# Kernel tuning notes

Hardware: AMD Instinct MI355X
Metric: run time of the kernel (lower is better)

## Reference

```python
import jax, jax.numpy as jnp
import numpy as np

NEG_SLOPE = 0.2  # negative_slope of LeakyReLU

def _leaky_relu(x):
    return jnp.where(x >= 0, x, NEG_SLOPE * x)

def setup_inputs() -> dict:
    key = jax.random.key(0)
    ks = jax.random.split(key, 8)
    n_s, n_t, n_edges = 100000, 25000, 1600000
    d_s_in = d_t_in = 256
    d_s_out = d_t_out = 256
    x_source = jax.random.normal(ks[0], (n_s, d_s_in), jnp.float32)
    x_target = jax.random.normal(ks[1], (n_t, d_t_in), jnp.float32)
    # sparse neighborhood N: [n_target, n_source], COO (row=target i, col=source j)
    edge_row = jax.random.randint(ks[2], (n_edges,), 0, n_t)
    edge_col = jax.random.randint(ks[3], (n_edges,), 0, n_s)
    n_vals = jax.random.uniform(ks[4], (n_edges,), jnp.float32)
    # learnable parameters (xavier-uniform-ish scale)
    w_s = jax.random.normal(ks[5], (d_s_in, d_t_out), jnp.float32) * 0.074  # [source_in, target_out]
    w_t = jax.random.normal(ks[6], (d_t_in, d_s_out), jnp.float32) * 0.074  # [target_in, source_out]
    att_weight = jax.random.normal(ks[7], (d_t_out + d_s_out,), jnp.float32) * 0.074
    return {"x_source": x_source, "x_target": x_target, "n_vals": n_vals,
            "w_s": w_s, "w_t": w_t, "att_weight": att_weight,
            "edge_row": edge_row, "edge_col": edge_col}

def reference(x_source, x_target, n_vals, w_s, w_t, att_weight, edge_row, edge_col):
    n_s = x_source.shape[0]
    n_t = x_target.shape[0]
    d_t_out = w_s.shape[1]  # target_out_channels (split point of att_weight)
    s_msg = x_source @ w_s  # [n_s, target_out]
    t_msg = x_target @ w_t  # [n_t, source_out]
    # e_ij = LeakyReLU([s_msg_j || t_msg_i] @ a); factor the linear part per node
    a1 = att_weight[:d_t_out]   # acts on s_msg part
    a2 = att_weight[d_t_out:]   # acts on t_msg part
    p_s = s_msg @ a1            # [n_s]
    p_t = t_msg @ a2            # [n_t]
    # f on the transposed edge (i'=source=col, j'=target=row) with permuted weight
    # [a2 || a1] gives p_t[row] + p_s[col]: identical per-edge scores as e.
    ev = _leaky_relu(p_s[edge_col] + p_t[edge_row])  # [E]
    # sparse_row_norm (softmax=False): divide by row sums
    rowsum_t = jax.ops.segment_sum(ev, edge_row, num_segments=n_t)  # rows of N
    rowsum_s = jax.ops.segment_sum(ev, edge_col, num_segments=n_s)  # rows of N^T
    att_s = ev / rowsum_t[edge_row]  # A_s, aligned with N
    att_t = ev / rowsum_s[edge_col]  # A_t, aligned with N^T
    # Hadamard with N values, then sparse-dense matmul (scatter-add)
    w_e = n_vals * att_s
    w_f = n_vals * att_t
    message_on_target = jax.ops.segment_sum(w_e[:, None] * s_msg[edge_col], edge_row, num_segments=n_t)  # Y_t
    message_on_source = jax.ops.segment_sum(w_f[:, None] * t_msg[edge_row], edge_col, num_segments=n_s)  # Y_s
    # update_func=None -> identity
    return message_on_source, message_on_target
```

## Files before the change

### kernel.cpp

```cpp
#include <hip/hip_runtime.h>

#define D 256

typedef float f32x4 __attribute__((ext_vector_type(4)));
typedef unsigned int u32x2 __attribute__((ext_vector_type(2)));
typedef short bf16x8 __attribute__((ext_vector_type(8)));
typedef float floatx4 __attribute__((ext_vector_type(4)));

__device__ __forceinline__ unsigned int rne_bf16(float f) {
    unsigned int u = __float_as_uint(f);
    return (u + 0x7FFFu + ((u >> 16) & 1u)) >> 16;
}

#define PROWS 32
#define PSTRIDE (D + 4)

__global__ __launch_bounds__(256) void fused_p_all(
        const float* __restrict__ xs, const float* __restrict__ ws,
        float* __restrict__ ps, unsigned short* __restrict__ xbs, int n_s, int nblk_s,
        const float* __restrict__ xt, const float* __restrict__ wt,
        float* __restrict__ pt, unsigned short* __restrict__ xbt, int n_t,
        const float* __restrict__ att) {
    __shared__ float sbuf[PROWS][PSTRIDE];
    const float* X; const float* W; float* p; unsigned short* xb;
    int M, att_off, row0;
    if (blockIdx.x < (unsigned)nblk_s) {
        X = xs; W = ws; p = ps; xb = xbs; M = n_s; att_off = 0;
        row0 = blockIdx.x * PROWS;
    } else {
        X = xt; W = wt; p = pt; xb = xbt; M = n_t; att_off = D;
        row0 = (blockIdx.x - nblk_s) * PROWS;
    }
    const int tid = threadIdx.x;
    for (int idx = tid; idx < PROWS * (D / 4); idx += 256) {
        int r = idx >> 6;
        int c4 = (idx & 63) * 4;
        int grow = row0 + r;
        int srcrow = grow < M ? grow : M - 1;
        *reinterpret_cast<float4*>(&sbuf[r][c4]) =
            *reinterpret_cast<const float4*>(X + (size_t)srcrow * D + c4);
    }
    __syncthreads();

    if (xb) {
        const int half = tid >> 7;
        const int c2 = (tid & 127) * 2;
        for (int r = half; r < PROWS; r += 2) {
            int row = row0 + r;
            if (row < M) {
                unsigned int u0 = rne_bf16(sbuf[r][c2]);
                unsigned int u1 = rne_bf16(sbuf[r][c2 + 1]);
                *reinterpret_cast<unsigned int*>(xb + (size_t)row * D + c2) =
                    (u1 << 16) | u0;
            }
        }
    }

    const int g = tid >> 6;
    const int l = tid & 63;
    const int r0 = g * 8;
    float acc[8][4];
    #pragma unroll
    for (int r = 0; r < 8; ++r)
        #pragma unroll
        for (int q = 0; q < 4; ++q) acc[r][q] = 0.f;

    const float* wbase = W + 4 * l;
    for (int k8 = 0; k8 < D; k8 += 8) {
        float4 wv[8];
        #pragma unroll
        for (int kk = 0; kk < 8; ++kk)
            wv[kk] = *reinterpret_cast<const float4*>(wbase + (size_t)(k8 + kk) * D);
        #pragma unroll
        for (int h = 0; h < 2; ++h) {
            float4 xv[8];
            #pragma unroll
            for (int r = 0; r < 8; ++r)
                xv[r] = *reinterpret_cast<const float4*>(&sbuf[r0 + r][k8 + 4 * h]);
            #pragma unroll
            for (int kk = 0; kk < 4; ++kk) {
                float4 w4 = wv[4 * h + kk];
                #pragma unroll
                for (int r = 0; r < 8; ++r) {
                    float xsc = (kk == 0) ? xv[r].x : (kk == 1) ? xv[r].y
                              : (kk == 2) ? xv[r].z : xv[r].w;
                    acc[r][0] = __fmaf_rn(xsc, w4.x, acc[r][0]);
                    acc[r][1] = __fmaf_rn(xsc, w4.y, acc[r][1]);
                    acc[r][2] = __fmaf_rn(xsc, w4.z, acc[r][2]);
                    acc[r][3] = __fmaf_rn(xsc, w4.w, acc[r][3]);
                }
            }
        }
    }
    __syncthreads();
    #pragma unroll
    for (int r = 0; r < 8; ++r)
        *reinterpret_cast<float4*>(&sbuf[r0 + r][4 * l]) =
            make_float4(acc[r][0], acc[r][1], acc[r][2], acc[r][3]);
    __syncthreads();
    if (tid < PROWS) {
        int row = row0 + tid;
        if (row < M) {
            float s = 0.f;
            const float* ap = att + att_off;
            for (int j = 0; j < D; ++j) s = __fmaf_rn(sbuf[tid][j], ap[j], s);
            p[row] = s;
        }
    }
}

__global__ void count_kernel(const int* __restrict__ er, const int* __restrict__ ec,
                             int* __restrict__ cnt_t, int* __restrict__ cnt_s, int ne) {
    int e = blockIdx.x * blockDim.x + threadIdx.x;
    int st = gridDim.x * blockDim.x;
    for (; e < ne; e += st) {
        atomicAdd(&cnt_t[er[e]], 1);
        atomicAdd(&cnt_s[ec[e]], 1);
    }
}

#define STILE 4096

__global__ __launch_bounds__(256) void scanA_kernel(
        const int* __restrict__ cnt_t, int n_t,
        const int* __restrict__ cnt_s, int n_s,
        int* __restrict__ tsum, int tilesT) {
    __shared__ int wsum[4];
    const int tid = threadIdx.x;
    const int* src; int n, base;
    if ((int)blockIdx.x < tilesT) { src = cnt_t; n = n_t; base = blockIdx.x * STILE; }
    else { src = cnt_s; n = n_s; base = (blockIdx.x - tilesT) * STILE; }
    int s = 0;
    for (int it = 0; it < STILE; it += 1024) {
        int idx = base + it + tid * 4;
        if (idx + 3 < n) {
            int4 v = *reinterpret_cast<const int4*>(src + idx);
            s += v.x + v.y + v.z + v.w;
        } else {
            #pragma unroll
            for (int k = 0; k < 4; ++k) if (idx + k < n) s += src[idx + k];
        }
    }
    #pragma unroll
    for (int o = 32; o > 0; o >>= 1) s += __shfl_xor(s, o, 64);
    if ((tid & 63) == 0) wsum[tid >> 6] = s;
    __syncthreads();
    if (tid == 0) tsum[blockIdx.x] = wsum[0] + wsum[1] + wsum[2] + wsum[3];
}

__global__ void scanB_kernel(int* __restrict__ tsum, int tilesT, int tilesS,
                             int* __restrict__ off_t, int n_t,
                             int* __restrict__ off_s, int n_s, int ne) {
    if (threadIdx.x == 0) {
        int run = 0;
        for (int i = 0; i < tilesT; ++i) { int v = tsum[i]; tsum[i] = run; run += v; }
        run = 0;
        for (int i = 0; i < tilesS; ++i) { int v = tsum[tilesT + i]; tsum[tilesT + i] = run; run += v; }
        off_t[n_t] = ne;
        off_s[n_s] = ne;
    }
}

__global__ __launch_bounds__(256) void scanC_kernel(
        const int* __restrict__ cnt_t, int n_t, int* __restrict__ off_t,
        const int* __restrict__ cnt_s, int n_s, int* __restrict__ off_s,
        const int* __restrict__ tsum, int tilesT) {
    __shared__ int wsum[4];
    __shared__ int s_carry;
    const int tid = threadIdx.x;
    const int lane = tid & 63, wv = tid >> 6;
    const int* src; int* dst; int n, base;
    if ((int)blockIdx.x < tilesT) { src = cnt_t; dst = off_t; n = n_t; base = blockIdx.x * STILE; }
    else { src = cnt_s; dst = off_s; n = n_s; base = (blockIdx.x - tilesT) * STILE; }
    if (tid == 0) s_carry = tsum[blockIdx.x];
    __syncthreads();
    for (int it = 0; it < STILE; it += 1024) {
        int idx = base + it + tid * 4;
        int4 v = make_int4(0, 0, 0, 0);
        if (idx + 3 < n) v = *reinterpret_cast<const int4*>(src + idx);
        else {
            if (idx < n)     v.x = src[idx];
            if (idx + 1 < n) v.y = src[idx + 1];
            if (idx + 2 < n) v.z = src[idx + 2];
        }
        int t4 = v.x + v.y + v.z + v.w;
        int x = t4;
        #pragma unroll
        for (int o = 1; o < 64; o <<= 1) {
            int y = __shfl_up(x, o, 64);
            if (lane >= o) x += y;
        }
        if (lane == 63) wsum[wv] = x;
        __syncthreads();
        int woff = 0;
        for (int w = 0; w < 4; ++w) if (w < wv) woff += wsum[w];
        int excl = s_carry + woff + x - t4;
        int4 outv;
        outv.x = excl;
        outv.y = excl + v.x;
        outv.z = excl + v.x + v.y;
        outv.w = excl + v.x + v.y + v.z;
        if (idx + 3 < n) *reinterpret_cast<int4*>(dst + idx) = outv;
        else {
            if (idx < n)     dst[idx] = outv.x;
            if (idx + 1 < n) dst[idx + 1] = outv.y;
            if (idx + 2 < n) dst[idx + 2] = outv.z;
        }
        __syncthreads();
        if (tid == 255) s_carry = excl + t4;
        __syncthreads();
    }
}

__global__ void fill_kernel(const int* __restrict__ er, const int* __restrict__ ec,
                            const int* __restrict__ off_t, const int* __restrict__ off_s,
                            int* __restrict__ cur_t, int* __restrict__ cur_s,
                            int* __restrict__ list_t, int* __restrict__ list_s, int ne) {
    int e = blockIdx.x * blockDim.x + threadIdx.x;
    int st = gridDim.x * blockDim.x;
    for (; e < ne; e += st) {
        int r = er[e];
        int p1 = atomicAdd(&cur_t[r], 1);
        list_t[off_t[r] + p1] = e;
        int c = ec[e];
        int p2 = atomicAdd(&cur_s[c], 1);
        list_s[off_s[c] + p2] = e;
    }
}

#define MAXD 160

__global__ __launch_bounds__(64) void rowsum_weight_all(
        const int* __restrict__ off_t, int* __restrict__ list_t,
        const int* __restrict__ ecol,
        const float* __restrict__ p_t, const float* __restrict__ p_s,
        float* __restrict__ wlist_t, int n_t,
        const int* __restrict__ off_s, int* __restrict__ list_s,
        const int* __restrict__ erow,
        float* __restrict__ wlist_s, int n_s,
        const float* __restrict__ nv) {
    __shared__ int raw[MAXD];
    __shared__ int so[MAXD];
    __shared__ float sev[MAXD];
    __shared__ float snv[MAXD];
    const int bid = blockIdx.x;
    const int* off; int* list; const int* other_idx;
    const float* p_own; const float* p_other; float* wlist; int row;
    if (bid < n_t) { off = off_t; list = list_t; other_idx = ecol;
                     p_own = p_t; p_other = p_s; wlist = wlist_t; row = bid; }
    else           { off = off_s; list = list_s; other_idx = erow;
                     p_own = p_s; p_other = p_t; wlist = wlist_s; row = bid - n_t; }
    const int lane = threadIdx.x;
    const int b = off[row];
    int deg = off[row + 1] - b;
    if (deg > MAXD) deg = MAXD;

    for (int i = lane; i < deg; i += 64)
        raw[i] = __builtin_nontemporal_load(list + b + i);
    __syncthreads();
    int myv[(MAXD + 63) / 64], myr[(MAXD + 63) / 64];
    #pragma unroll
    for (int c = 0; c < (MAXD + 63) / 64; ++c) {
        int i = lane + c * 64;
        if (i < deg) {
            int v = raw[i];
            int rank = 0;
            for (int j = 0; j < deg; ++j) rank += (raw[j] < v);
            myv[c] = v; myr[c] = rank;
        }
    }
    __syncthreads();
    #pragma unroll
    for (int c = 0; c < (MAXD + 63) / 64; ++c) {
        int i = lane + c * 64;
        if (i < deg) raw[myr[c]] = myv[c];
    }
    __syncthreads();
    const float po = p_own[row];
    for (int i = lane; i < deg; i += 64) {
        int e = raw[i];
        int o = other_idx[e];
        so[i] = o;
        float t = __fadd_rn(p_other[o], po);
        sev[i] = (t >= 0.f) ? t : __fmul_rn(0.2f, t);
        snv[i] = __builtin_nontemporal_load(nv + e);
    }
    __syncthreads();
    float rs = 0.f;
    for (int i = 0; i < deg; ++i) rs = __fadd_rn(rs, sev[i]);
    for (int i = lane; i < deg; i += 64) {
        list[b + i]  = so[i];
        wlist[b + i] = __fmul_rn(snv[i], __fdiv_rn(sev[i], rs));
    }
}

__global__ __launch_bounds__(256) void gather_all_bf16(
        const int* __restrict__ off_t, const int* __restrict__ olist_t,
        const float* __restrict__ wlist_t, const unsigned short* __restrict__ xb_s,
        float* __restrict__ out_tgt, unsigned short* __restrict__ aggb_tgt, int n_t,
        const int* __restrict__ off_s, const int* __restrict__ olist_s,
        const float* __restrict__ wlist_s, const unsigned short* __restrict__ xb_t,
        float* __restrict__ out_src, unsigned short* __restrict__ aggb_src, int n_s) {
    const int gid = blockIdx.x * 4 + (threadIdx.x >> 6);
    if (gid >= n_t + n_s) return;
    const int lane = threadIdx.x & 63;
    const int* off; const int* ol; const float* wl;
    const unsigned short* xo; float* out; unsigned short* aggb; int row;
    if (gid < n_t) { off = off_t; ol = olist_t; wl = wlist_t;
                     xo = xb_s; out = out_tgt; aggb = aggb_tgt; row = gid; }
    else           { off = off_s; ol = olist_s; wl = wlist_s;
                     xo = xb_t; out = out_src; aggb = aggb_src; row = gid - n_t; }
    const int b = off[row];
    const int end = off[row + 1];
    const size_t eoff = (size_t)lane * 4;

    float ax = 0.f, ay = 0.f, az = 0.f, aw = 0.f;
    for (int cs = b; cs < end; cs += 64) {
        const int cn = min(64, end - cs);
        int o_l = 0; float w_l = 0.f;
        if (lane < cn) {
            o_l = __builtin_nontemporal_load(ol + cs + lane);
            w_l = __builtin_nontemporal_load(wl + cs + lane);
        }
        int e = 0;
        for (; e + 16 <= cn; e += 16) {
            float w[16]; uint2 xv[16];
            #pragma unroll
            for (int u = 0; u < 16; ++u) {
                int o = __shfl(o_l, e + u, 64);
                w[u] = __shfl(w_l, e + u, 64);
                xv[u] = *reinterpret_cast<const uint2*>(xo + (size_t)o * D + eoff);
            }
            #pragma unroll
            for (int u = 0; u < 16; ++u) {
                float x0 = __uint_as_float(xv[u].x << 16);
                float x1 = __uint_as_float(xv[u].x & 0xFFFF0000u);
                float x2 = __uint_as_float(xv[u].y << 16);
                float x3 = __uint_as_float(xv[u].y & 0xFFFF0000u);
                ax = fmaf(w[u], x0, ax); ay = fmaf(w[u], x1, ay);
                az = fmaf(w[u], x2, az); aw = fmaf(w[u], x3, aw);
            }
        }
        for (; e < cn; ++e) {
            int o = __shfl(o_l, e, 64);
            float w = __shfl(w_l, e, 64);
            uint2 xv = *reinterpret_cast<const uint2*>(xo + (size_t)o * D + eoff);
            float x0 = __uint_as_float(xv.x << 16);
            float x1 = __uint_as_float(xv.x & 0xFFFF0000u);
            float x2 = __uint_as_float(xv.y << 16);
            float x3 = __uint_as_float(xv.y & 0xFFFF0000u);
            ax = fmaf(w, x0, ax); ay = fmaf(w, x1, ay);
            az = fmaf(w, x2, az); aw = fmaf(w, x3, aw);
        }
    }
    if (aggb) {
        u32x2 pk = { (rne_bf16(ay) << 16) | rne_bf16(ax),
                     (rne_bf16(aw) << 16) | rne_bf16(az) };
        __builtin_nontemporal_store(pk,
            reinterpret_cast<u32x2*>(aggb + (size_t)row * D + eoff));
    } else {
        f32x4 r = {ax, ay, az, aw};
        __builtin_nontemporal_store(r,
            reinterpret_cast<f32x4*>(out + (size_t)row * D + eoff));
    }
}

#define GR 64

__global__ __launch_bounds__(256) void band_mfma_all(
        const unsigned short* __restrict__ aggb_s, float* __restrict__ out_s,
        int nblk_s, int Ms, const float* __restrict__ W_for_s,
        const unsigned short* __restrict__ aggb_t, float* __restrict__ out_t,
        int Mt, const float* __restrict__ W_for_t) {
    __shared__ unsigned short WT[256][40];
    const unsigned short* A; float* Cout; const float* W; int M, base;
    if (blockIdx.x < (unsigned)nblk_s) {
        A = aggb_s; Cout = out_s; W = W_for_s; M = Ms; base = blockIdx.x * GR;
    } else {
        A = aggb_t; Cout = out_t; W = W_for_t; M = Mt;
        base = (blockIdx.x - nblk_s) * GR;
    }
    const int tid = threadIdx.x;
    const int wv = tid >> 6;
    const int l  = tid & 63;
    const int lr = l & 15;
    const int lg = l >> 4;
    const int wrow0 = base + wv * 16;

    floatx4 acc[16];
    #pragma unroll
    for (int ct = 0; ct < 16; ++ct) acc[ct] = (floatx4){0.f, 0.f, 0.f, 0.f};

    for (int ks = 0; ks < 8; ++ks) {
        const int k0 = ks * 32;
        __syncthreads();
        for (int idx = tid; idx < 32 * 256; idx += 256) {
            int c = idx & 255, kr = idx >> 8;
            WT[c][kr] = (unsigned short)rne_bf16(W[(size_t)(k0 + kr) * D + c]);
        }
        __syncthreads();
        int arow = wrow0 + lr;
        if (arow >= M) arow = M - 1;
        bf16x8 af = *reinterpret_cast<const bf16x8*>(A + (size_t)arow * D + k0 + 8 * lg);
        #pragma unroll
        for (int ct = 0; ct < 16; ++ct) {
            bf16x8 bf = *reinterpret_cast<const bf16x8*>(&WT[ct * 16 + lr][8 * lg]);
            acc[ct] = __builtin_amdgcn_mfma_f32_16x16x32_bf16(af, bf, acc[ct], 0, 0, 0);
        }
    }
    #pragma unroll
    for (int ct = 0; ct < 16; ++ct) {
        int col = ct * 16 + lr;
        #pragma unroll
        for (int j = 0; j < 4; ++j) {
            int row = wrow0 + lg * 4 + j;
            if (row < M) Cout[(size_t)row * D + col] = acc[ct][j];
        }
    }
}

#define BAND 32
#define KT 8

__global__ __launch_bounds__(256) void band_gemm_all(
        float* __restrict__ Cs, const float* __restrict__ Bs_w, int nblk_s, int Ms,
        float* __restrict__ Ct, const float* __restrict__ Bt_w, int Mt) {
    __shared__ float Xs[BAND][D];
    __shared__ float Bs[KT][D];
    float* C; const float* B; int M, base_row;
    if (blockIdx.x < (unsigned)nblk_s) { C = Cs; B = Bs_w; M = Ms; base_row = blockIdx.x * BAND; }
    else { C = Ct; B = Bt_w; M = Mt; base_row = (blockIdx.x - nblk_s) * BAND; }
    const int tid = threadIdx.x;
    const int r0 = (tid >> 5) * 4;
    const int cA = (tid & 31) * 4;

    for (int s = tid; s < BAND * (D / 4); s += 256) {
        int row = s >> 6;
        int c4 = (s & 63) * 4;
        int grow = base_row + row;
        int srow = grow < M ? grow : M - 1;
        f32x4 v = __builtin_nontemporal_load(
            reinterpret_cast<const f32x4*>(C + (size_t)srow * D + c4));
        *reinterpret_cast<f32x4*>(&Xs[row][c4]) = v;
    }

    float acc[4][8];
    #pragma unroll
    for (int i = 0; i < 4; ++i)
        #pragma unroll
        for (int j = 0; j < 8; ++j) acc[i][j] = 0.f;

    for (int kt = 0; kt < D; kt += KT) {
        __syncthreads();
        for (int s = tid; s < KT * (D / 4); s += 256) {
            int row = s >> 6;
            int c4 = (s & 63) * 4;
            *reinterpret_cast<float4*>(&Bs[row][c4]) =
                *reinterpret_cast<const float4*>(B + (size_t)(kt + row) * D + c4);
        }
        __syncthreads();
        #pragma unroll
        for (int k4 = 0; k4 < KT; k4 += 4) {
            float4 av[4];
            #pragma unroll
            for (int i = 0; i < 4; ++i)
                av[i] = *reinterpret_cast<const float4*>(&Xs[r0 + i][kt + k4]);
            #pragma unroll
            for (int kk = 0; kk < 4; ++kk) {
                float4 blo = *reinterpret_cast<const float4*>(&Bs[k4 + kk][cA]);
                float4 bhi = *reinterpret_cast<const float4*>(&Bs[k4 + kk][cA + 128]);
                #pragma unroll
                for (int i = 0; i < 4; ++i) {
                    float a = (kk == 0) ? av[i].x : (kk == 1) ? av[i].y
                            : (kk == 2) ? av[i].z : av[i].w;
                    acc[i][0] = fmaf(a, blo.x, acc[i][0]);
                    acc[i][1] = fmaf(a, blo.y, acc[i][1]);
                    acc[i][2] = fmaf(a, blo.z, acc[i][2]);
                    acc[i][3] = fmaf(a, blo.w, acc[i][3]);
                    acc[i][4] = fmaf(a, bhi.x, acc[i][4]);
                    acc[i][5] = fmaf(a, bhi.y, acc[i][5]);
                    acc[i][6] = fmaf(a, bhi.z, acc[i][6]);
                    acc[i][7] = fmaf(a, bhi.w, acc[i][7]);
                }
            }
        }
    }
    #pragma unroll
    for (int i = 0; i < 4; ++i) {
        int row = base_row + r0 + i;
        if (row < M) {
            float* cp = C + (size_t)row * D;
            f32x4 lo = {acc[i][0], acc[i][1], acc[i][2], acc[i][3]};
            f32x4 hi = {acc[i][4], acc[i][5], acc[i][6], acc[i][7]};
            __builtin_nontemporal_store(lo, reinterpret_cast<f32x4*>(cp + cA));
            __builtin_nontemporal_store(hi, reinterpret_cast<f32x4*>(cp + cA + 128));
        }
    }
}

extern "C" void kernel_launch(void* const* d_in, const int* in_sizes, int n_in,
                              void* d_out, int out_size, void* d_ws, size_t ws_size,
                              hipStream_t stream) {
    const float* x_s = (const float*)d_in[0];
    const float* x_t = (const float*)d_in[1];
    const float* nv  = (const float*)d_in[2];
    const float* w_s = (const float*)d_in[3];
    const float* w_t = (const float*)d_in[4];
    const float* att = (const float*)d_in[5];
    const int* erow  = (const int*)d_in[6];
    const int* ecol  = (const int*)d_in[7];

    const int n_s = in_sizes[0] / D;
    const int n_t = in_sizes[1] / D;
    const int ne  = in_sizes[6];

    float* p_s      = (float*)d_ws;
    float* p_t      = p_s + n_s;
    float* wlist_t  = p_t + n_t;
    float* wlist_s  = wlist_t + ne;
    int* cnt_t  = (int*)(wlist_s + ne);
    int* cnt_s  = cnt_t + n_t;
    int* cur_t  = cnt_s + n_s;
    int* cur_s  = cur_t + n_t;
    int* off_t  = cur_s + n_s;
    int* off_s  = off_t + (n_t + 1);
    int* tsum   = off_s + (n_s + 1);
    int* list_t = tsum + 64;
    int* list_s = list_t + ne;
    unsigned short* xb_s = (unsigned short*)(list_s + ne);
    unsigned short* xb_t = xb_s + (size_t)n_s * D;
    unsigned short* aggb_src = xb_t + (size_t)n_t * D;
    unsigned short* aggb_tgt = aggb_src + (size_t)n_s * D;
    size_t need_bf16 = (size_t)((char*)(xb_t + (size_t)n_t * D) - (char*)d_ws);
    size_t need_mfma = (size_t)((char*)(aggb_tgt + (size_t)n_t * D) - (char*)d_ws);
    const bool use_bf16 = ws_size >= need_bf16;
    const bool use_mfma = ws_size >= need_mfma;

    float* out_src = (float*)d_out;
    float* out_tgt = out_src + (size_t)n_s * D;

    (void)hipMemsetAsync(cnt_t, 0, 2 * (size_t)(n_t + n_s) * sizeof(int), stream);

    const int pblk_s = (n_s + PROWS - 1) / PROWS;
    const int pblk_t = (n_t + PROWS - 1) / PROWS;
    fused_p_all<<<pblk_s + pblk_t, 256, 0, stream>>>(
        x_s, w_s, p_s, use_bf16 ? xb_s : nullptr, n_s, pblk_s,
        x_t, w_t, p_t, use_bf16 ? xb_t : nullptr, n_t, att);

    count_kernel<<<2048, 256, 0, stream>>>(erow, ecol, cnt_t, cnt_s, ne);

    const int tilesT = (n_t + STILE - 1) / STILE;
    const int tilesS = (n_s + STILE - 1) / STILE;
    scanA_kernel<<<tilesT + tilesS, 256, 0, stream>>>(cnt_t, n_t, cnt_s, n_s,
                                                      tsum, tilesT);
    scanB_kernel<<<1, 64, 0, stream>>>(tsum, tilesT, tilesS,
                                       off_t, n_t, off_s, n_s, ne);
    scanC_kernel<<<tilesT + tilesS, 256, 0, stream>>>(cnt_t, n_t, off_t,
                                                      cnt_s, n_s, off_s,
                                                      tsum, tilesT);

    fill_kernel<<<2048, 256, 0, stream>>>(erow, ecol, off_t, off_s, cur_t, cur_s,
                                          list_t, list_s, ne);

    rowsum_weight_all<<<n_t + n_s, 64, 0, stream>>>(off_t, list_t, ecol, p_t, p_s,
                                                    wlist_t, n_t,
                                                    off_s, list_s, erow,
                                                    wlist_s, n_s, nv);

    int rows = n_t + n_s;
    gather_all_bf16<<<(rows + 3) / 4, 256, 0, stream>>>(
        off_t, list_t, wlist_t, xb_s, out_tgt, use_mfma ? aggb_tgt : nullptr, n_t,
        off_s, list_s, wlist_s, xb_t, out_src, use_mfma ? aggb_src : nullptr, n_s);

    if (use_mfma) {
        const int mblk_s = (n_s + GR - 1) / GR;
        const int mblk_t = (n_t + GR - 1) / GR;
        band_mfma_all<<<mblk_s + mblk_t, 256, 0, stream>>>(
            aggb_src, out_src, mblk_s, n_s, w_t,
            aggb_tgt, out_tgt, n_t, w_s);
    } else {
        const int gblk_s = (n_s + BAND - 1) / BAND;
        const int gblk_t = (n_t + BAND - 1) / BAND;
        band_gemm_all<<<gblk_s + gblk_t, 256, 0, stream>>>(out_src, w_t, gblk_s, n_s,
                                                           out_tgt, w_s, n_t);
    }
}
```

Before: 994.6 us.

## Fuse per-row attention weight computation into the gather kernel

Merges the rowsum/weight kernel and the bf16 gather kernel into one per-row kernel. The sorted neighbor indices and normalized weights now stay in shared memory and feed the gather directly, so the separate wlist arrays and the rewrite of list_t/list_s to global memory are gone. The cost is that the gather now runs with 64-thread blocks, one row per block, instead of four rows per 256-thread block. That may lower occupancy or scheduling efficiency for the bandwidth-heavy gather.

```diff
diff --git a/kernel.cpp b/kernel.cpp
--- a/kernel.cpp
+++ b/kernel.cpp
@@ -230,26 +230,31 @@
 
 #define MAXD 160
 
-__global__ __launch_bounds__(64) void rowsum_weight_all(
-        const int* __restrict__ off_t, int* __restrict__ list_t,
+__global__ __launch_bounds__(64) void rowsum_gather_all(
+        const int* __restrict__ off_t, const int* __restrict__ list_t,
         const int* __restrict__ ecol,
         const float* __restrict__ p_t, const float* __restrict__ p_s,
-        float* __restrict__ wlist_t, int n_t,
-        const int* __restrict__ off_s, int* __restrict__ list_s,
+        const unsigned short* __restrict__ xb_s,
+        float* __restrict__ out_tgt, unsigned short* __restrict__ aggb_tgt, int n_t,
+        const int* __restrict__ off_s, const int* __restrict__ list_s,
         const int* __restrict__ erow,
-        float* __restrict__ wlist_s, int n_s,
+        const unsigned short* __restrict__ xb_t,
+        float* __restrict__ out_src, unsigned short* __restrict__ aggb_src, int n_s,
         const float* __restrict__ nv) {
     __shared__ int raw[MAXD];
     __shared__ int so[MAXD];
     __shared__ float sev[MAXD];
     __shared__ float snv[MAXD];
     const int bid = blockIdx.x;
-    const int* off; int* list; const int* other_idx;
-    const float* p_own; const float* p_other; float* wlist; int row;
+    const int* off; const int* list; const int* other_idx;
+    const float* p_own; const float* p_other;
+    const unsigned short* xo; float* out; unsigned short* aggb; int row;
     if (bid < n_t) { off = off_t; list = list_t; other_idx = ecol;
-                     p_own = p_t; p_other = p_s; wlist = wlist_t; row = bid; }
+                     p_own = p_t; p_other = p_s; xo = xb_s;
+                     out = out_tgt; aggb = aggb_tgt; row = bid; }
     else           { off = off_s; list = list_s; other_idx = erow;
-                     p_own = p_s; p_other = p_t; wlist = wlist_s; row = bid - n_t; }
+                     p_own = p_s; p_other = p_t; xo = xb_t;
+                     out = out_src; aggb = aggb_src; row = bid - n_t; }
     const int lane = threadIdx.x;
     const int b = off[row];
     int deg = off[row + 1] - b;
@@ -288,40 +293,16 @@
     __syncthreads();
     float rs = 0.f;
     for (int i = 0; i < deg; ++i) rs = __fadd_rn(rs, sev[i]);
-    for (int i = lane; i < deg; i += 64) {
-        list[b + i]  = so[i];
-        wlist[b + i] = __fmul_rn(snv[i], __fdiv_rn(sev[i], rs));
-    }
-}
-
-__global__ __launch_bounds__(256) void gather_all_bf16(
-        const int* __restrict__ off_t, const int* __restrict__ olist_t,
-        const float* __restrict__ wlist_t, const unsigned short* __restrict__ xb_s,
-        float* __restrict__ out_tgt, unsigned short* __restrict__ aggb_tgt, int n_t,
-        const int* __restrict__ off_s, const int* __restrict__ olist_s,
-        const float* __restrict__ wlist_s, const unsigned short* __restrict__ xb_t,
-        float* __restrict__ out_src, unsigned short* __restrict__ aggb_src, int n_s) {
-    const int gid = blockIdx.x * 4 + (threadIdx.x >> 6);
-    if (gid >= n_t + n_s) return;
-    const int lane = threadIdx.x & 63;
-    const int* off; const int* ol; const float* wl;
-    const unsigned short* xo; float* out; unsigned short* aggb; int row;
-    if (gid < n_t) { off = off_t; ol = olist_t; wl = wlist_t;
-                     xo = xb_s; out = out_tgt; aggb = aggb_tgt; row = gid; }
-    else           { off = off_s; ol = olist_s; wl = wlist_s;
-                     xo = xb_t; out = out_src; aggb = aggb_src; row = gid - n_t; }
-    const int b = off[row];
-    const int end = off[row + 1];
+    for (int i = lane; i < deg; i += 64)
+        sev[i] = __fmul_rn(snv[i], __fdiv_rn(sev[i], rs));
+    __syncthreads();
+
     const size_t eoff = (size_t)lane * 4;
-
     float ax = 0.f, ay = 0.f, az = 0.f, aw = 0.f;
-    for (int cs = b; cs < end; cs += 64) {
-        const int cn = min(64, end - cs);
+    for (int cs = 0; cs < deg; cs += 64) {
+        const int cn = min(64, deg - cs);
         int o_l = 0; float w_l = 0.f;
-        if (lane < cn) {
-            o_l = __builtin_nontemporal_load(ol + cs + lane);
-            w_l = __builtin_nontemporal_load(wl + cs + lane);
-        }
+        if (lane < cn) { o_l = so[cs + lane]; w_l = sev[cs + lane]; }
         int e = 0;
         for (; e + 16 <= cn; e += 16) {
             float w[16]; uint2 xv[16];
@@ -516,9 +497,7 @@
 
     float* p_s      = (float*)d_ws;
     float* p_t      = p_s + n_s;
-    float* wlist_t  = p_t + n_t;
-    float* wlist_s  = wlist_t + ne;
-    int* cnt_t  = (int*)(wlist_s + ne);
+    int* cnt_t  = (int*)(p_t + n_t);
     int* cnt_s  = cnt_t + n_t;
     int* cur_t  = cnt_s + n_s;
     int* cur_s  = cur_t + n_t;
@@ -562,15 +541,11 @@
     fill_kernel<<<2048, 256, 0, stream>>>(erow, ecol, off_t, off_s, cur_t, cur_s,
                                           list_t, list_s, ne);
 
-    rowsum_weight_all<<<n_t + n_s, 64, 0, stream>>>(off_t, list_t, ecol, p_t, p_s,
-                                                    wlist_t, n_t,
-                                                    off_s, list_s, erow,
-                                                    wlist_s, n_s, nv);
-
-    int rows = n_t + n_s;
-    gather_all_bf16<<<(rows + 3) / 4, 256, 0, stream>>>(
-        off_t, list_t, wlist_t, xb_s, out_tgt, use_mfma ? aggb_tgt : nullptr, n_t,
-        off_s, list_s, wlist_s, xb_t, out_src, use_mfma ? aggb_src : nullptr, n_s);
+    rowsum_gather_all<<<n_t + n_s, 64, 0, stream>>>(
+        off_t, list_t, ecol, p_t, p_s, xb_s,
+        out_tgt, use_mfma ? aggb_tgt : nullptr, n_t,
+        off_s, list_s, erow, xb_t,
+        out_src, use_mfma ? aggb_src : nullptr, n_s, nv);
 
     if (use_mfma) {
         const int mblk_s = (n_s + GR - 1) / GR;
```

New measurement: 950.7 us. 4.4% less time.
